# Optimization experiments

Hardware: AMD Instinct MI355X
Metric: run time of the kernel (lower is better)

The kernel has to match this reference:

```python
import jax, jax.numpy as jnp
import numpy as np

N = 100000        # nodes
E = 1600000       # directed edges (avg degree 16)
EMB = 32          # emb_hidden_dim
HID = 16          # hidden
Q = 0.25          # magnetic charge
NUM_SYMP = 15
BY = 4            # num_birthyear_disc


def _norm(edge_index, edge_weight):
    # Magnetic Laplacian, 'sym' normalization, lambda_max=2:
    # L_hat(u,v) = -deg^{-1/2}(u) * A_sym(u,v) * deg^{-1/2}(v) * exp(i*theta(u,v)),
    # theta = 2*pi*q*(A - A^T); diagonal of scaled L_hat is 0.
    src, dst = edge_index[0], edge_index[1]
    src2 = jnp.concatenate([src, dst])
    dst2 = jnp.concatenate([dst, src])
    sym_w = jnp.concatenate([edge_weight, edge_weight]) * 0.5
    theta = (2.0 * jnp.pi * Q) * jnp.concatenate([edge_weight, -edge_weight])
    deg = jax.ops.segment_sum(sym_w, dst2, num_segments=N)
    dinv = jnp.where(deg > 0, jax.lax.rsqrt(jnp.where(deg > 0, deg, 1.0)), 0.0)
    norm = dinv[src2] * sym_w * dinv[dst2]
    return src2, dst2, -norm * jnp.cos(theta), -norm * jnp.sin(theta)


def _cmatvec(src2, dst2, a_re, a_im, xr, xi):
    # complex sparse matvec: (A_re + i A_im)(x_re + i x_im)
    xr_s, xi_s = xr[src2], xi[src2]
    yr = jax.ops.segment_sum(a_re[:, None] * xr_s - a_im[:, None] * xi_s, dst2, num_segments=N)
    yi = jax.ops.segment_sum(a_re[:, None] * xi_s + a_im[:, None] * xr_s, dst2, num_segments=N)
    return yr, yi


def _magnet_conv(xr, xi, adj, W, b):
    # Chebyshev recursion T0=x, T1=L_hat x, T2=2 L_hat T1 - T0; out = sum_k T_k @ W[k] + b
    src2, dst2, a_re, a_im = adj
    out_r = xr @ W[0]
    out_i = xi @ W[0]
    t1r, t1i = _cmatvec(src2, dst2, a_re, a_im, xr, xi)
    out_r = out_r + t1r @ W[1]
    out_i = out_i + t1i @ W[1]
    t2r, t2i = _cmatvec(src2, dst2, a_re, a_im, t1r, t1i)
    t2r = 2.0 * t2r - xr
    t2i = 2.0 * t2i - xi
    out_r = out_r + t2r @ W[2]
    out_i = out_i + t2i @ W[2]
    return out_r + b, out_i + b


def setup_inputs() -> dict:
    key = jax.random.key(0)
    ks = jax.random.split(key, 12)
    birth = jax.random.randint(ks[0], (N,), 0, BY)
    gender = jax.random.randint(ks[1], (N,), 0, 2)
    symp = jax.random.randint(ks[2], (N, NUM_SYMP), 0, 3)
    x = jnp.concatenate([
        jax.nn.one_hot(birth, BY, dtype=jnp.int32),
        gender[:, None].astype(jnp.int32),
        symp.astype(jnp.int32),
    ], axis=1)  # [N, 20]
    edge_index = jax.random.randint(ks[3], (2, E), 0, N)
    edge_weight = jnp.ones((E,), jnp.float32)
    s = 0.1
    return {
        'x': x,
        'edge_index': edge_index,
        'edge_weight': edge_weight,
        'birth_tab': jax.random.normal(ks[4], (BY, EMB), jnp.float32) * s,
        'gender_tab': jax.random.normal(ks[5], (2, EMB), jnp.float32) * s,
        'symp_tab': jax.random.normal(ks[6], (NUM_SYMP, 3, EMB), jnp.float32) * s,
        'W1': jax.random.normal(ks[7], (3, EMB, HID), jnp.float32) * s,
        'b1': jnp.zeros((HID,), jnp.float32),
        'W2': jax.random.normal(ks[8], (3, HID, HID), jnp.float32) * s,
        'b2': jnp.zeros((HID,), jnp.float32),
        'Wc': jax.random.normal(ks[9], (2 * HID, 2 * HID), jnp.float32) * s,  # Conv1d k=1 (out,in)
        'bc': jnp.zeros((2 * HID,), jnp.float32),
        'Wl': jax.random.normal(ks[10], (2 * HID, 1), jnp.float32) * s,
        'bl': jnp.zeros((1,), jnp.float32),
    }


def reference(x, edge_index, edge_weight, birth_tab, gender_tab, symp_tab,
              W1, b1, W2, b2, Wc, bc, Wl, bl):
    # embedding gathers + mean fusion
    birth_idx = jnp.argmax(x[:, :BY] == 1, axis=1)
    birth_e = birth_tab[birth_idx]                              # [N, EMB]
    gender_e = gender_tab[x[:, BY]]                             # [N, EMB]
    symp_e = symp_tab[jnp.arange(NUM_SYMP)[None, :], x[:, -NUM_SYMP:]]  # [N, 15, EMB]
    feat = jnp.mean(symp_e, axis=1)
    h = (birth_e + gender_e + feat) / 3.0                       # [N, EMB]
    # complex Chebyshev spectral graph conv layers
    adj = _norm(edge_index, edge_weight)
    re, im = _magnet_conv(h, h, adj, W1, b1)
    re, im = _magnet_conv(re, im, adj, W2, b2)
    z = jnp.concatenate([re, im], axis=-1)                      # [N, 2*HID]
    z = z @ Wc.T + bc                                           # Conv1d kernel_size=1
    y = z @ Wl + bl                                             # Linear(2*HID, 1)
    return y[:, 0]
```

## Files before the change

kernel.cpp:

```cpp
#include <hip/hip_runtime.h>
#include <hip/hip_fp16.h>
#include <math.h>

static constexpr float PI2Q = 1.57079632679489662f;
#define CSH 9
#define CROWS 512
#define MAXKEY 256

__device__ __forceinline__ float2 h2f_bits(int b) {
  __half2 h = *reinterpret_cast<__half2*>(&b);
  return __half22float2(h);
}
__device__ __forceinline__ int f2h_bits(float a, float b) {
  __half2 h = __floats2half2_rn(a, b);
  return *reinterpret_cast<int*>(&h);
}

__global__ void k_weff(const float* __restrict__ Wc, const float* __restrict__ bc,
                       const float* __restrict__ Wl, const float* __restrict__ bl,
                       float* __restrict__ weff) {
  int k = threadIdx.x;
  if (k < 32) {
    float s = 0.f;
    #pragma unroll
    for (int j = 0; j < 32; ++j) s += Wc[j * 32 + k] * Wl[j];
    weff[k] = s;
  } else if (k == 32) {
    float s = 0.f;
    for (int j = 0; j < 32; ++j) s += bc[j] * Wl[j];
    weff[32] = s + bl[0];
  }
}

__global__ __launch_bounds__(256) void k_embed(
    const int* __restrict__ x, const float* __restrict__ btab,
    const float* __restrict__ gtab, const float* __restrict__ stab,
    const float* __restrict__ W1, const float* __restrict__ b1,
    float* __restrict__ PQ, __half2* __restrict__ PQh, float* __restrict__ o0, int n) {
  __shared__ float sm[3184];
  int tid = threadIdx.x;
  for (int t = tid; t < 1536; t += 256) sm[t] = W1[t];
  if (tid < 16) sm[1536 + tid] = b1[tid];
  for (int t = tid; t < 128; t += 256) sm[1552 + t] = btab[t];
  for (int t = tid; t < 64; t += 256) sm[1680 + t] = gtab[t];
  for (int t = tid; t < 1440; t += 256) sm[1744 + t] = stab[t];
  __syncthreads();
  int i = blockIdx.x * 256 + tid;
  if (i >= n) return;
  int xr[20];
  #pragma unroll
  for (int j = 0; j < 20; ++j) xr[j] = x[i * 20 + j];
  int bi = 0;
  #pragma unroll
  for (int j = 3; j >= 0; --j) if (xr[j] == 1) bi = j;
  int g = xr[4];
  float h[32];
  #pragma unroll
  for (int f = 0; f < 32; ++f) {
    float s = 0.f;
    #pragma unroll
    for (int j = 0; j < 15; ++j) s += sm[1744 + j * 96 + xr[5 + j] * 32 + f];
    h[f] = (sm[1552 + bi * 32 + f] + sm[1680 + g * 32 + f] + s * (1.f / 15.f)) * (1.f / 3.f);
  }
  #pragma unroll
  for (int f = 0; f < 16; ++f) {
    float o = sm[1536 + f], p = 0.f, q = 0.f;
    #pragma unroll
    for (int k = 0; k < 32; ++k) {
      float hk = h[k];
      o = fmaf(hk, sm[k * 16 + f], o);
      p = fmaf(hk, sm[512 + k * 16 + f], p);
      q = fmaf(hk, sm[1024 + k * 16 + f], q);
    }
    o0[i * 16 + f] = o;
    PQ[i * 32 + 2 * f] = p;
    PQ[i * 32 + 2 * f + 1] = q;
    PQh[(size_t)i * 16 + f] = __floats2half2_rn(p, q);
  }
}

__global__ __launch_bounds__(256) void k_rhist(const int* __restrict__ ei, int* __restrict__ rcnt,
                                               int E_) {
  __shared__ int h[MAXKEY * 8];
  int tid = threadIdx.x;
  for (int t = tid; t < MAXKEY * 8; t += 256) h[t] = 0;
  __syncthreads();
  int slot = tid & 7;
  int stride = gridDim.x * 256;
  for (int e = blockIdx.x * 256 + tid; e < E_; e += stride) {
    int s = ei[e], d = ei[E_ + e];
    atomicAdd(&h[(d >> CSH) * 8 + slot], 1);
    atomicAdd(&h[(s >> CSH) * 8 + slot], 1);
  }
  __syncthreads();
  for (int t = tid; t < MAXKEY; t += 256) {
    int sum = 0;
    #pragma unroll
    for (int j = 0; j < 8; ++j) sum += h[t * 8 + j];
    if (sum) atomicAdd(&rcnt[t], sum);
  }
}

__global__ void k_rbase(const int* __restrict__ rcnt, int* __restrict__ rbase, int* __restrict__ rcur,
                        int nkey) {
  if (threadIdx.x == 0) {
    int run = 0;
    for (int r = 0; r < nkey; ++r) { rbase[r] = run; rcur[r] = run; run += rcnt[r]; }
    rbase[nkey] = run;
  }
}

__global__ __launch_bounds__(256) void k_bucket(const int* __restrict__ ei, const float* __restrict__ ew,
                                                int* __restrict__ rcur, int* __restrict__ brow,
                                                int2* __restrict__ bsw, int E_) {
  __shared__ int lcnt[MAXKEY];
  __shared__ int gbase[MAXKEY];
  int tid = threadIdx.x;
  lcnt[tid] = 0;
  __syncthreads();
  int e0 = blockIdx.x * 2048;
  int s[8], d[8], wb[8], kA[8], kB[8], la[8], lb[8];
  #pragma unroll
  for (int j = 0; j < 8; ++j) {
    int e = e0 + j * 256 + tid;
    if (e < E_) {
      s[j] = ei[e]; d[j] = ei[E_ + e]; wb[j] = __float_as_int(ew[e]);
      kA[j] = d[j] >> CSH;
      kB[j] = s[j] >> CSH;
      la[j] = atomicAdd(&lcnt[kA[j]], 1);
      lb[j] = atomicAdd(&lcnt[kB[j]], 1);
    } else {
      kA[j] = -1; kB[j] = -1; s[j] = 0; d[j] = 0; wb[j] = 0; la[j] = 0; lb[j] = 0;
    }
  }
  __syncthreads();
  gbase[tid] = lcnt[tid] ? atomicAdd(&rcur[tid], lcnt[tid]) : 0;
  __syncthreads();
  #pragma unroll
  for (int j = 0; j < 8; ++j) {
    if (kA[j] >= 0) {
      int pA = gbase[kA[j]] + la[j];
      brow[pA] = d[j];
      bsw[pA] = make_int2(s[j], wb[j]);
      int pB = gbase[kB[j]] + lb[j];
      brow[pB] = s[j];
      bsw[pB] = make_int2(d[j] | (int)0x80000000, wb[j]);
    }
  }
}

__global__ __launch_bounds__(1024) void k_chunkdeg(const int* __restrict__ brow, const int2* __restrict__ bsw,
                                                   const int* __restrict__ rbase, int* __restrict__ rowp,
                                                   float* __restrict__ dinv, int n, int nkey) {
  __shared__ int hist[CROWS];
  __shared__ float wsum[CROWS];
  __shared__ int pref[CROWS];
  int c = blockIdx.x;
  int base = c << CSH;
  int rows = min(CROWS, n - base);
  int tid = threadIdx.x;
  if (tid < CROWS) { hist[tid] = 0; wsum[tid] = 0.f; }
  __syncthreads();
  int k0 = rbase[c], k1 = rbase[c + 1];
  for (int k = k0 + tid; k < k1; k += 1024) {
    int rl = brow[k] - base;
    atomicAdd(&hist[rl], 1);
    atomicAdd(&wsum[rl], __int_as_float(bsw[k].y));
  }
  __syncthreads();
  if (tid < CROWS) pref[tid] = hist[tid];
  __syncthreads();
  for (int off = 1; off < CROWS; off <<= 1) {
    int t = (tid < CROWS && tid >= off) ? pref[tid - off] : 0;
    __syncthreads();
    if (tid < CROWS) pref[tid] += t;
    __syncthreads();
  }
  if (tid < rows) {
    rowp[base + tid] = k0 + pref[tid] - hist[tid];
    float dg = 0.5f * wsum[tid];
    dinv[base + tid] = (dg > 0.f) ? rsqrtf(dg) : 0.f;
  }
  if (c == 0 && tid == 0) rowp[n] = rbase[nkey];
}

__global__ __launch_bounds__(1024) void k_chunkplace(const int* __restrict__ brow, const int2* __restrict__ bsw,
                                                     const int* __restrict__ rbase, const int* __restrict__ rowp,
                                                     const float* __restrict__ dinv, int2* __restrict__ recs,
                                                     int n) {
  __shared__ int cur[CROWS];
  __shared__ float dloc[CROWS];
  int c = blockIdx.x;
  int base = c << CSH;
  int rows = min(CROWS, n - base);
  int tid = threadIdx.x;
  if (tid < rows) { cur[tid] = rowp[base + tid]; dloc[tid] = dinv[base + tid]; }
  __syncthreads();
  int k0 = rbase[c], k1 = rbase[c + 1];
  for (int k = k0 + tid; k < k1; k += 1024) {
    int rl = brow[k] - base;
    int2 p = bsw[k];
    int s = p.x & 0x7fffffff;
    float w = __int_as_float(p.y);
    float nrm = dloc[rl] * 0.5f * w * dinv[s];
    float sn, cs;
    sincosf(PI2Q * w, &sn, &cs);
    float ar = -nrm * cs;
    float ai = (p.x < 0) ? nrm * sn : -nrm * sn;
    int pos = atomicAdd(&cur[rl], 1);
    recs[pos] = make_int2(p.x, f2h_bits(ar, ai));
  }
}

__global__ __launch_bounds__(256, 8) void k_hop_sym(
    const int* __restrict__ rowp, const int2* __restrict__ recs,
    const __half2* __restrict__ PQh, __half2* __restrict__ Uh, float* __restrict__ AB, int n) {
  int wid = (blockIdx.x * 256 + threadIdx.x) >> 6;
  if (wid >= n) return;
  int lane = threadIdx.x & 63;
  int fq = lane & 3, su = lane >> 2;
  int rs = rowp[wid], rend = rowp[wid + 1];
  float aA[4] = {0.f, 0.f, 0.f, 0.f}, aB[4] = {0.f, 0.f, 0.f, 0.f};
  float aC[4] = {0.f, 0.f, 0.f, 0.f}, aD[4] = {0.f, 0.f, 0.f, 0.f};
  const long long* rq = reinterpret_cast<const long long*>(recs);
  const int4* Pq = reinterpret_cast<const int4*>(PQh);
  for (int k = rs + su; k < rend; k += 16) {
    long long r0 = __builtin_nontemporal_load(rq + k);
    int s = ((int)r0) & 0x7fffffff;
    float2 a = h2f_bits((int)(r0 >> 32));
    float wm = a.x - a.y, wp = a.x + a.y;
    int4 v = Pq[(size_t)s * 4 + fq];
    float2 x0 = h2f_bits(v.x), x1 = h2f_bits(v.y), x2 = h2f_bits(v.z), x3 = h2f_bits(v.w);
    aA[0] = fmaf(wm, x0.x, aA[0]); aB[0] = fmaf(wp, x0.x, aB[0]);
    aC[0] = fmaf(wm, x0.y, aC[0]); aD[0] = fmaf(wp, x0.y, aD[0]);
    aA[1] = fmaf(wm, x1.x, aA[1]); aB[1] = fmaf(wp, x1.x, aB[1]);
    aC[1] = fmaf(wm, x1.y, aC[1]); aD[1] = fmaf(wp, x1.y, aD[1]);
    aA[2] = fmaf(wm, x2.x, aA[2]); aB[2] = fmaf(wp, x2.x, aB[2]);
    aC[2] = fmaf(wm, x2.y, aC[2]); aD[2] = fmaf(wp, x2.y, aD[2]);
    aA[3] = fmaf(wm, x3.x, aA[3]); aB[3] = fmaf(wp, x3.x, aB[3]);
    aC[3] = fmaf(wm, x3.y, aC[3]); aD[3] = fmaf(wp, x3.y, aD[3]);
  }
  #pragma unroll
  for (int j = 0; j < 4; ++j) {
    aA[j] += __shfl_xor(aA[j], 4); aA[j] += __shfl_xor(aA[j], 8);
    aA[j] += __shfl_xor(aA[j], 16); aA[j] += __shfl_xor(aA[j], 32);
    aB[j] += __shfl_xor(aB[j], 4); aB[j] += __shfl_xor(aB[j], 8);
    aB[j] += __shfl_xor(aB[j], 16); aB[j] += __shfl_xor(aB[j], 32);
    aC[j] += __shfl_xor(aC[j], 4); aC[j] += __shfl_xor(aC[j], 8);
    aC[j] += __shfl_xor(aC[j], 16); aC[j] += __shfl_xor(aC[j], 32);
    aD[j] += __shfl_xor(aD[j], 4); aD[j] += __shfl_xor(aD[j], 8);
    aD[j] += __shfl_xor(aD[j], 16); aD[j] += __shfl_xor(aD[j], 32);
  }
  if (lane < 4) {
    *reinterpret_cast<float4*>(AB + wid * 32 + 8 * fq) = make_float4(aA[0], aB[0], aA[1], aB[1]);
    *reinterpret_cast<float4*>(AB + wid * 32 + 8 * fq + 4) = make_float4(aA[2], aB[2], aA[3], aB[3]);
    int4 hv;
    hv.x = f2h_bits(aC[0], aD[0]); hv.y = f2h_bits(aC[1], aD[1]);
    hv.z = f2h_bits(aC[2], aD[2]); hv.w = f2h_bits(aC[3], aD[3]);
    *reinterpret_cast<int4*>(Uh + (size_t)wid * 16 + 4 * fq) = hv;
  }
}

template <int MODE>
__global__ __launch_bounds__(256, 8) void k_hop_full(
    const int* __restrict__ rowp, const int2* __restrict__ recs,
    const __half2* __restrict__ Xh, float* __restrict__ Y, __half2* __restrict__ Yh,
    const float* __restrict__ o0, const float* __restrict__ AB, const float* __restrict__ PQ,
    const float* __restrict__ D, const float* __restrict__ weff, int n) {
  int wid = (blockIdx.x * 256 + threadIdx.x) >> 6;
  if (wid >= n) return;
  int lane = threadIdx.x & 63;
  int fq = lane & 3, su = lane >> 2;
  int rs = rowp[wid], rend = rowp[wid + 1];
  float aR[4] = {0.f, 0.f, 0.f, 0.f}, aI[4] = {0.f, 0.f, 0.f, 0.f};
  const long long* rq = reinterpret_cast<const long long*>(recs);
  const int4* Xq = reinterpret_cast<const int4*>(Xh);
  for (int k = rs + su; k < rend; k += 16) {
    long long r0 = __builtin_nontemporal_load(rq + k);
    int s = ((int)r0) & 0x7fffffff;
    float2 a = h2f_bits((int)(r0 >> 32));
    int4 v = Xq[(size_t)s * 4 + fq];
    float2 x0 = h2f_bits(v.x), x1 = h2f_bits(v.y), x2 = h2f_bits(v.z), x3 = h2f_bits(v.w);
    aR[0] = fmaf(a.x, x0.x, aR[0]); aR[0] = fmaf(-a.y, x0.y, aR[0]);
    aI[0] = fmaf(a.x, x0.y, aI[0]); aI[0] = fmaf(a.y, x0.x, aI[0]);
    aR[1] = fmaf(a.x, x1.x, aR[1]); aR[1] = fmaf(-a.y, x1.y, aR[1]);
    aI[1] = fmaf(a.x, x1.y, aI[1]); aI[1] = fmaf(a.y, x1.x, aI[1]);
    aR[2] = fmaf(a.x, x2.x, aR[2]); aR[2] = fmaf(-a.y, x2.y, aR[2]);
    aI[2] = fmaf(a.x, x2.y, aI[2]); aI[2] = fmaf(a.y, x2.x, aI[2]);
    aR[3] = fmaf(a.x, x3.x, aR[3]); aR[3] = fmaf(-a.y, x3.y, aR[3]);
    aI[3] = fmaf(a.x, x3.y, aI[3]); aI[3] = fmaf(a.y, x3.x, aI[3]);
  }
  #pragma unroll
  for (int j = 0; j < 4; ++j) {
    aR[j] += __shfl_xor(aR[j], 4); aR[j] += __shfl_xor(aR[j], 8);
    aR[j] += __shfl_xor(aR[j], 16); aR[j] += __shfl_xor(aR[j], 32);
    aI[j] += __shfl_xor(aI[j], 4); aI[j] += __shfl_xor(aI[j], 8);
    aI[j] += __shfl_xor(aI[j], 16); aI[j] += __shfl_xor(aI[j], 32);
  }
  if (MODE == 2) {
    float c = 0.f;
    if (lane < 4) {
      float4 d0 = *reinterpret_cast<const float4*>(D + wid * 32 + 8 * fq);
      float4 d1 = *reinterpret_cast<const float4*>(D + wid * 32 + 8 * fq + 4);
      float4 w0 = *reinterpret_cast<const float4*>(weff + 4 * fq);
      float4 w1 = *reinterpret_cast<const float4*>(weff + 16 + 4 * fq);
      c  = (d0.x + 2.f * aR[0]) * w0.x + (d0.y + 2.f * aI[0]) * w1.x;
      c += (d0.z + 2.f * aR[1]) * w0.y + (d0.w + 2.f * aI[1]) * w1.y;
      c += (d1.x + 2.f * aR[2]) * w0.z + (d1.y + 2.f * aI[2]) * w1.z;
      c += (d1.z + 2.f * aR[3]) * w0.w + (d1.w + 2.f * aI[3]) * w1.w;
    }
    c += __shfl_xor(c, 1); c += __shfl_xor(c, 2);
    if (lane == 0) Y[wid] = c + weff[32];
  } else if (lane < 4) {
    if (MODE == 0) {
      *reinterpret_cast<float4*>(Y + wid * 32 + 8 * fq) = make_float4(aR[0], aI[0], aR[1], aI[1]);
      *reinterpret_cast<float4*>(Y + wid * 32 + 8 * fq + 4) = make_float4(aR[2], aI[2], aR[3], aI[3]);
    } else {
      float4 o = *reinterpret_cast<const float4*>(o0 + wid * 16 + 4 * fq);
      float4 ab0 = *reinterpret_cast<const float4*>(AB + wid * 32 + 8 * fq);
      float4 ab1 = *reinterpret_cast<const float4*>(AB + wid * 32 + 8 * fq + 4);
      float4 pq0 = *reinterpret_cast<const float4*>(PQ + wid * 32 + 8 * fq);
      float4 pq1 = *reinterpret_cast<const float4*>(PQ + wid * 32 + 8 * fq + 4);
      float zr0 = o.x + ab0.x + 2.f * aR[0] - pq0.y;
      float zi0 = o.x + ab0.y + 2.f * aI[0] - pq0.y;
      float zr1 = o.y + ab0.z + 2.f * aR[1] - pq0.w;
      float zi1 = o.y + ab0.w + 2.f * aI[1] - pq0.w;
      float zr2 = o.z + ab1.x + 2.f * aR[2] - pq1.y;
      float zi2 = o.z + ab1.y + 2.f * aI[2] - pq1.y;
      float zr3 = o.w + ab1.z + 2.f * aR[3] - pq1.w;
      float zi3 = o.w + ab1.w + 2.f * aI[3] - pq1.w;
      *reinterpret_cast<float4*>(Y + wid * 32 + 8 * fq) = make_float4(zr0, zi0, zr1, zi1);
      *reinterpret_cast<float4*>(Y + wid * 32 + 8 * fq + 4) = make_float4(zr2, zi2, zr3, zi3);
      int4 hv;
      hv.x = f2h_bits(zr0, zi0); hv.y = f2h_bits(zr1, zi1);
      hv.z = f2h_bits(zr2, zi2); hv.w = f2h_bits(zr3, zi3);
      *reinterpret_cast<int4*>(Yh + (size_t)wid * 16 + 4 * fq) = hv;
    }
  }
}

__global__ __launch_bounds__(256) void k_d2(const float* __restrict__ X2, const float* __restrict__ T1,
                                            const float* __restrict__ W2g, const float* __restrict__ b2g,
                                            __half2* __restrict__ U2h, float* __restrict__ D, int n) {
  __shared__ float sm[1040];
  int tid = threadIdx.x;
  for (int t = tid; t < 768; t += 256) sm[t] = W2g[t];
  if (tid < 16) sm[768 + tid] = b2g[tid];
  __syncthreads();
  if (tid < 256) sm[784 + tid] = sm[tid] - sm[512 + tid];
  __syncthreads();
  int i = blockIdx.x * 256 + tid;
  if (i >= n) return;
  float re[16], im[16], tr[16], ti[16];
  #pragma unroll
  for (int k = 0; k < 16; ++k) {
    float2 a = *reinterpret_cast<const float2*>(X2 + i * 32 + 2 * k);
    re[k] = a.x; im[k] = a.y;
    float2 b = *reinterpret_cast<const float2*>(T1 + i * 32 + 2 * k);
    tr[k] = b.x; ti[k] = b.y;
  }
  #pragma unroll
  for (int f = 0; f < 16; ++f) {
    float ur = 0.f, ui = 0.f;
    float dr = sm[768 + f], di = sm[768 + f];
    #pragma unroll
    for (int k = 0; k < 16; ++k) {
      float w2 = sm[512 + k * 16 + f];
      float w1 = sm[256 + k * 16 + f];
      float w02 = sm[784 + k * 16 + f];
      ur = fmaf(tr[k], w2, ur);
      ui = fmaf(ti[k], w2, ui);
      dr = fmaf(re[k], w02, dr); dr = fmaf(tr[k], w1, dr);
      di = fmaf(im[k], w02, di); di = fmaf(ti[k], w1, di);
    }
    U2h[(size_t)i * 16 + f] = __floats2half2_rn(ur, ui);
    *reinterpret_cast<float2*>(D + i * 32 + 2 * f) = make_float2(dr, di);
  }
}

extern "C" void kernel_launch(void* const* d_in, const int* in_sizes, int n_in,
                              void* d_out, int out_size, void* d_ws, size_t ws_size,
                              hipStream_t stream) {
  const int* x = (const int*)d_in[0];
  const int* ei = (const int*)d_in[1];
  const float* ew = (const float*)d_in[2];
  const float* btab = (const float*)d_in[3];
  const float* gtab = (const float*)d_in[4];
  const float* stab = (const float*)d_in[5];
  const float* W1 = (const float*)d_in[6];
  const float* b1 = (const float*)d_in[7];
  const float* W2 = (const float*)d_in[8];
  const float* b2 = (const float*)d_in[9];
  const float* Wc = (const float*)d_in[10];
  const float* bc = (const float*)d_in[11];
  const float* Wl = (const float*)d_in[12];
  const float* bl = (const float*)d_in[13];
  float* yout = (float*)d_out;

  const int N_ = in_sizes[0] / 20;
  const int E_ = in_sizes[1] / 2;
  const int M_ = 2 * E_;
  const int nkey = (N_ + CROWS - 1) >> CSH;

  size_t off = 0;
  auto take = [&](size_t bytes) -> void* {
    void* p = (char*)d_ws + off;
    off += (bytes + 255) & ~(size_t)255;
    return p;
  };
  float* PQ   = (float*)take((size_t)N_ * 32 * 4);
  float* o0   = (float*)take((size_t)N_ * 16 * 4);
  float* Ubuf = (float*)take((size_t)N_ * 32 * 4);
  float* ABuf = (float*)take((size_t)N_ * 32 * 4);
  float* X2   = (float*)take((size_t)N_ * 32 * 4);
  float* dinv = (float*)take((size_t)N_ * 4);
  int* rowp   = (int*)take((size_t)(N_ + 1) * 4);
  float* weff = (float*)take(64 * 4);
  int* rcnt   = (int*)take(MAXKEY * 4);
  int* rbase  = (int*)take((MAXKEY + 1) * 4);
  int* rcur   = (int*)take(MAXKEY * 4);
  int* brow   = (int*)take((size_t)M_ * 4);
  int2* bsw   = (int2*)take((size_t)M_ * 8);
  int2* recs  = (int2*)take((size_t)M_ * 8);
  (void)ws_size; (void)n_in; (void)out_size;

  __half2* PQh = (__half2*)brow;
  __half2* Uh  = (__half2*)((char*)brow + (size_t)N_ * 64);
  __half2* X2h = (__half2*)bsw;
  __half2* U2h = (__half2*)((char*)bsw + (size_t)N_ * 64);

  int nbN = (N_ + 255) / 256;
  int nbH = (N_ + 3) / 4;
  int nbB = (E_ + 2047) / 2048;

  hipMemsetAsync(rcnt, 0, MAXKEY * 4, stream);

  k_weff<<<1, 64, 0, stream>>>(Wc, bc, Wl, bl, weff);

  k_rhist<<<512, 256, 0, stream>>>(ei, rcnt, E_);
  k_rbase<<<1, 64, 0, stream>>>(rcnt, rbase, rcur, nkey);
  k_bucket<<<nbB, 256, 0, stream>>>(ei, ew, rcur, brow, bsw, E_);
  k_chunkdeg<<<nkey, 1024, 0, stream>>>(brow, bsw, rbase, rowp, dinv, N_, nkey);
  k_chunkplace<<<nkey, 1024, 0, stream>>>(brow, bsw, rbase, rowp, dinv, recs, N_);

  k_embed<<<nbN, 256, 0, stream>>>(x, btab, gtab, stab, W1, b1, PQ, PQh, o0, N_);

  k_hop_sym<<<nbH, 256, 0, stream>>>(rowp, recs, PQh, Uh, ABuf, N_);
  k_hop_full<1><<<nbH, 256, 0, stream>>>(rowp, recs, Uh, X2, X2h, o0, ABuf, PQ,
                                         nullptr, nullptr, N_);
  k_hop_full<0><<<nbH, 256, 0, stream>>>(rowp, recs, X2h, Ubuf, nullptr, nullptr,
                                         nullptr, nullptr, nullptr, nullptr, N_);
  k_d2<<<nbN, 256, 0, stream>>>(X2, Ubuf, W2, b2, U2h, ABuf, N_);
  k_hop_full<2><<<nbH, 256, 0, stream>>>(rowp, recs, U2h, yout, nullptr, nullptr,
                                         nullptr, nullptr, ABuf, weff, N_);
}
```

Measured before the change: 452.2 us.

## Make hop kernels persistent with software-prefetched edge records for next row

Converts the four SpMM hop kernels from one-wavefront-per-row launches into a persistent grid of 2048 blocks where each wavefront strides over rows. While the current row is processed, it prefetches the next row's rowp bounds and first three edge records, and it issues the first three feature gathers of each row together to raise memory-level parallelism. The aim is to hide gather latency and launch/tail overhead. The cost is extra registers, masked dummy gathers for short rows, and fewer resident wavefronts if the grid is too small for the device.

```diff
diff --git a/kernel.cpp b/kernel.cpp
--- a/kernel.cpp
+++ b/kernel.cpp
@@ -6,6 +6,7 @@
 #define CSH 9
 #define CROWS 512
 #define MAXKEY 256
+#define HOPB 2048
 
 __device__ __forceinline__ float2 h2f_bits(int b) {
   __half2 h = *reinterpret_cast<__half2*>(&b);
@@ -214,50 +215,99 @@
 
 __global__ __launch_bounds__(256, 8) void k_hop_sym(
     const int* __restrict__ rowp, const int2* __restrict__ recs,
-    const __half2* __restrict__ PQh, __half2* __restrict__ Uh, float* __restrict__ AB, int n) {
-  int wid = (blockIdx.x * 256 + threadIdx.x) >> 6;
-  if (wid >= n) return;
+    const __half2* __restrict__ PQh, __half2* __restrict__ Uh, float* __restrict__ AB,
+    int n, int M, int W) {
+  int w = (blockIdx.x * 256 + threadIdx.x) >> 6;
+  if (w >= n) return;
   int lane = threadIdx.x & 63;
   int fq = lane & 3, su = lane >> 2;
-  int rs = rowp[wid], rend = rowp[wid + 1];
-  float aA[4] = {0.f, 0.f, 0.f, 0.f}, aB[4] = {0.f, 0.f, 0.f, 0.f};
-  float aC[4] = {0.f, 0.f, 0.f, 0.f}, aD[4] = {0.f, 0.f, 0.f, 0.f};
   const long long* rq = reinterpret_cast<const long long*>(recs);
   const int4* Pq = reinterpret_cast<const int4*>(PQh);
-  for (int k = rs + su; k < rend; k += 16) {
-    long long r0 = __builtin_nontemporal_load(rq + k);
-    int s = ((int)r0) & 0x7fffffff;
-    float2 a = h2f_bits((int)(r0 >> 32));
-    float wm = a.x - a.y, wp = a.x + a.y;
-    int4 v = Pq[(size_t)s * 4 + fq];
-    float2 x0 = h2f_bits(v.x), x1 = h2f_bits(v.y), x2 = h2f_bits(v.z), x3 = h2f_bits(v.w);
-    aA[0] = fmaf(wm, x0.x, aA[0]); aB[0] = fmaf(wp, x0.x, aB[0]);
-    aC[0] = fmaf(wm, x0.y, aC[0]); aD[0] = fmaf(wp, x0.y, aD[0]);
-    aA[1] = fmaf(wm, x1.x, aA[1]); aB[1] = fmaf(wp, x1.x, aB[1]);
-    aC[1] = fmaf(wm, x1.y, aC[1]); aD[1] = fmaf(wp, x1.y, aD[1]);
-    aA[2] = fmaf(wm, x2.x, aA[2]); aB[2] = fmaf(wp, x2.x, aB[2]);
-    aC[2] = fmaf(wm, x2.y, aC[2]); aD[2] = fmaf(wp, x2.y, aD[2]);
-    aA[3] = fmaf(wm, x3.x, aA[3]); aB[3] = fmaf(wp, x3.x, aB[3]);
-    aC[3] = fmaf(wm, x3.y, aC[3]); aD[3] = fmaf(wp, x3.y, aD[3]);
-  }
-  #pragma unroll
-  for (int j = 0; j < 4; ++j) {
-    aA[j] += __shfl_xor(aA[j], 4); aA[j] += __shfl_xor(aA[j], 8);
-    aA[j] += __shfl_xor(aA[j], 16); aA[j] += __shfl_xor(aA[j], 32);
-    aB[j] += __shfl_xor(aB[j], 4); aB[j] += __shfl_xor(aB[j], 8);
-    aB[j] += __shfl_xor(aB[j], 16); aB[j] += __shfl_xor(aB[j], 32);
-    aC[j] += __shfl_xor(aC[j], 4); aC[j] += __shfl_xor(aC[j], 8);
-    aC[j] += __shfl_xor(aC[j], 16); aC[j] += __shfl_xor(aC[j], 32);
-    aD[j] += __shfl_xor(aD[j], 4); aD[j] += __shfl_xor(aD[j], 8);
-    aD[j] += __shfl_xor(aD[j], 16); aD[j] += __shfl_xor(aD[j], 32);
-  }
-  if (lane < 4) {
-    *reinterpret_cast<float4*>(AB + wid * 32 + 8 * fq) = make_float4(aA[0], aB[0], aA[1], aB[1]);
-    *reinterpret_cast<float4*>(AB + wid * 32 + 8 * fq + 4) = make_float4(aA[2], aB[2], aA[3], aB[3]);
-    int4 hv;
-    hv.x = f2h_bits(aC[0], aD[0]); hv.y = f2h_bits(aC[1], aD[1]);
-    hv.z = f2h_bits(aC[2], aD[2]); hv.w = f2h_bits(aC[3], aD[3]);
-    *reinterpret_cast<int4*>(Uh + (size_t)wid * 16 + 4 * fq) = hv;
+  int Mm1 = M - 1;
+
+  int r = w;
+  int rs = rowp[r], re = rowp[r + 1];
+  int k0 = rs + su;
+  long long c0 = __builtin_nontemporal_load(rq + min(k0, Mm1));
+  long long c1 = __builtin_nontemporal_load(rq + min(k0 + 16, Mm1));
+  long long c2 = __builtin_nontemporal_load(rq + min(k0 + 32, Mm1));
+
+  while (true) {
+    int rn = r + W;
+    int nrs = 0, nre = 0;
+    if (rn < n) { nrs = rowp[rn]; nre = rowp[rn + 1]; }
+
+    int s0 = ((int)c0) & 0x7fffffff;
+    int s1 = ((int)c1) & 0x7fffffff;
+    int s2 = ((int)c2) & 0x7fffffff;
+    float2 a0 = h2f_bits((int)(c0 >> 32));
+    float2 a1 = h2f_bits((int)(c1 >> 32));
+    float2 a2 = h2f_bits((int)(c2 >> 32));
+    if (k0 >= re)      { a0 = make_float2(0.f, 0.f); }
+    if (k0 + 16 >= re) { a1 = make_float2(0.f, 0.f); s1 = s0; }
+    if (k0 + 32 >= re) { a2 = make_float2(0.f, 0.f); s2 = s0; }
+
+    int4 g0 = Pq[(size_t)s0 * 4 + fq];
+    int4 g1 = Pq[(size_t)s1 * 4 + fq];
+    int4 g2 = Pq[(size_t)s2 * 4 + fq];
+
+    long long n0 = 0, n1 = 0, n2 = 0;
+    int nk0 = nrs + su;
+    if (rn < n) {
+      n0 = __builtin_nontemporal_load(rq + min(nk0, Mm1));
+      n1 = __builtin_nontemporal_load(rq + min(nk0 + 16, Mm1));
+      n2 = __builtin_nontemporal_load(rq + min(nk0 + 32, Mm1));
+    }
+
+    float aA[4] = {0.f, 0.f, 0.f, 0.f}, aB[4] = {0.f, 0.f, 0.f, 0.f};
+    float aC[4] = {0.f, 0.f, 0.f, 0.f}, aD[4] = {0.f, 0.f, 0.f, 0.f};
+    #define SYM_FMA(aa, vv)                                                              \
+    {                                                                                    \
+      float wm = aa.x - aa.y, wp = aa.x + aa.y;                                          \
+      float2 x0 = h2f_bits(vv.x), x1 = h2f_bits(vv.y), x2 = h2f_bits(vv.z), x3 = h2f_bits(vv.w); \
+      aA[0] = fmaf(wm, x0.x, aA[0]); aB[0] = fmaf(wp, x0.x, aB[0]);                      \
+      aC[0] = fmaf(wm, x0.y, aC[0]); aD[0] = fmaf(wp, x0.y, aD[0]);                      \
+      aA[1] = fmaf(wm, x1.x, aA[1]); aB[1] = fmaf(wp, x1.x, aB[1]);                      \
+      aC[1] = fmaf(wm, x1.y, aC[1]); aD[1] = fmaf(wp, x1.y, aD[1]);                      \
+      aA[2] = fmaf(wm, x2.x, aA[2]); aB[2] = fmaf(wp, x2.x, aB[2]);                      \
+      aC[2] = fmaf(wm, x2.y, aC[2]); aD[2] = fmaf(wp, x2.y, aD[2]);                      \
+      aA[3] = fmaf(wm, x3.x, aA[3]); aB[3] = fmaf(wp, x3.x, aB[3]);                      \
+      aC[3] = fmaf(wm, x3.y, aC[3]); aD[3] = fmaf(wp, x3.y, aD[3]);                      \
+    }
+    SYM_FMA(a0, g0);
+    SYM_FMA(a1, g1);
+    SYM_FMA(a2, g2);
+    for (int k = rs + 48 + su; k < re; k += 16) {
+      long long rr = __builtin_nontemporal_load(rq + k);
+      int ss = ((int)rr) & 0x7fffffff;
+      float2 aa = h2f_bits((int)(rr >> 32));
+      int4 gg = Pq[(size_t)ss * 4 + fq];
+      SYM_FMA(aa, gg);
+    }
+    #undef SYM_FMA
+
+    #pragma unroll
+    for (int j = 0; j < 4; ++j) {
+      aA[j] += __shfl_xor(aA[j], 4); aA[j] += __shfl_xor(aA[j], 8);
+      aA[j] += __shfl_xor(aA[j], 16); aA[j] += __shfl_xor(aA[j], 32);
+      aB[j] += __shfl_xor(aB[j], 4); aB[j] += __shfl_xor(aB[j], 8);
+      aB[j] += __shfl_xor(aB[j], 16); aB[j] += __shfl_xor(aB[j], 32);
+      aC[j] += __shfl_xor(aC[j], 4); aC[j] += __shfl_xor(aC[j], 8);
+      aC[j] += __shfl_xor(aC[j], 16); aC[j] += __shfl_xor(aC[j], 32);
+      aD[j] += __shfl_xor(aD[j], 4); aD[j] += __shfl_xor(aD[j], 8);
+      aD[j] += __shfl_xor(aD[j], 16); aD[j] += __shfl_xor(aD[j], 32);
+    }
+    if (lane < 4) {
+      *reinterpret_cast<float4*>(AB + r * 32 + 8 * fq) = make_float4(aA[0], aB[0], aA[1], aB[1]);
+      *reinterpret_cast<float4*>(AB + r * 32 + 8 * fq + 4) = make_float4(aA[2], aB[2], aA[3], aB[3]);
+      int4 hv;
+      hv.x = f2h_bits(aC[0], aD[0]); hv.y = f2h_bits(aC[1], aD[1]);
+      hv.z = f2h_bits(aC[2], aD[2]); hv.w = f2h_bits(aC[3], aD[3]);
+      *reinterpret_cast<int4*>(Uh + (size_t)r * 16 + 4 * fq) = hv;
+    }
+    if (rn >= n) break;
+    r = rn; rs = nrs; re = nre; k0 = nk0;
+    c0 = n0; c1 = n1; c2 = n2;
   }
 }
 
@@ -266,76 +316,124 @@
     const int* __restrict__ rowp, const int2* __restrict__ recs,
     const __half2* __restrict__ Xh, float* __restrict__ Y, __half2* __restrict__ Yh,
     const float* __restrict__ o0, const float* __restrict__ AB, const float* __restrict__ PQ,
-    const float* __restrict__ D, const float* __restrict__ weff, int n) {
-  int wid = (blockIdx.x * 256 + threadIdx.x) >> 6;
-  if (wid >= n) return;
+    const float* __restrict__ D, const float* __restrict__ weff, int n, int M, int W) {
+  int w = (blockIdx.x * 256 + threadIdx.x) >> 6;
+  if (w >= n) return;
   int lane = threadIdx.x & 63;
   int fq = lane & 3, su = lane >> 2;
-  int rs = rowp[wid], rend = rowp[wid + 1];
-  float aR[4] = {0.f, 0.f, 0.f, 0.f}, aI[4] = {0.f, 0.f, 0.f, 0.f};
   const long long* rq = reinterpret_cast<const long long*>(recs);
   const int4* Xq = reinterpret_cast<const int4*>(Xh);
-  for (int k = rs + su; k < rend; k += 16) {
-    long long r0 = __builtin_nontemporal_load(rq + k);
-    int s = ((int)r0) & 0x7fffffff;
-    float2 a = h2f_bits((int)(r0 >> 32));
-    int4 v = Xq[(size_t)s * 4 + fq];
-    float2 x0 = h2f_bits(v.x), x1 = h2f_bits(v.y), x2 = h2f_bits(v.z), x3 = h2f_bits(v.w);
-    aR[0] = fmaf(a.x, x0.x, aR[0]); aR[0] = fmaf(-a.y, x0.y, aR[0]);
-    aI[0] = fmaf(a.x, x0.y, aI[0]); aI[0] = fmaf(a.y, x0.x, aI[0]);
-    aR[1] = fmaf(a.x, x1.x, aR[1]); aR[1] = fmaf(-a.y, x1.y, aR[1]);
-    aI[1] = fmaf(a.x, x1.y, aI[1]); aI[1] = fmaf(a.y, x1.x, aI[1]);
-    aR[2] = fmaf(a.x, x2.x, aR[2]); aR[2] = fmaf(-a.y, x2.y, aR[2]);
-    aI[2] = fmaf(a.x, x2.y, aI[2]); aI[2] = fmaf(a.y, x2.x, aI[2]);
-    aR[3] = fmaf(a.x, x3.x, aR[3]); aR[3] = fmaf(-a.y, x3.y, aR[3]);
-    aI[3] = fmaf(a.x, x3.y, aI[3]); aI[3] = fmaf(a.y, x3.x, aI[3]);
-  }
-  #pragma unroll
-  for (int j = 0; j < 4; ++j) {
-    aR[j] += __shfl_xor(aR[j], 4); aR[j] += __shfl_xor(aR[j], 8);
-    aR[j] += __shfl_xor(aR[j], 16); aR[j] += __shfl_xor(aR[j], 32);
-    aI[j] += __shfl_xor(aI[j], 4); aI[j] += __shfl_xor(aI[j], 8);
-    aI[j] += __shfl_xor(aI[j], 16); aI[j] += __shfl_xor(aI[j], 32);
-  }
-  if (MODE == 2) {
-    float c = 0.f;
-    if (lane < 4) {
-      float4 d0 = *reinterpret_cast<const float4*>(D + wid * 32 + 8 * fq);
-      float4 d1 = *reinterpret_cast<const float4*>(D + wid * 32 + 8 * fq + 4);
-      float4 w0 = *reinterpret_cast<const float4*>(weff + 4 * fq);
-      float4 w1 = *reinterpret_cast<const float4*>(weff + 16 + 4 * fq);
-      c  = (d0.x + 2.f * aR[0]) * w0.x + (d0.y + 2.f * aI[0]) * w1.x;
-      c += (d0.z + 2.f * aR[1]) * w0.y + (d0.w + 2.f * aI[1]) * w1.y;
-      c += (d1.x + 2.f * aR[2]) * w0.z + (d1.y + 2.f * aI[2]) * w1.z;
-      c += (d1.z + 2.f * aR[3]) * w0.w + (d1.w + 2.f * aI[3]) * w1.w;
-    }
-    c += __shfl_xor(c, 1); c += __shfl_xor(c, 2);
-    if (lane == 0) Y[wid] = c + weff[32];
-  } else if (lane < 4) {
-    if (MODE == 0) {
-      *reinterpret_cast<float4*>(Y + wid * 32 + 8 * fq) = make_float4(aR[0], aI[0], aR[1], aI[1]);
-      *reinterpret_cast<float4*>(Y + wid * 32 + 8 * fq + 4) = make_float4(aR[2], aI[2], aR[3], aI[3]);
-    } else {
-      float4 o = *reinterpret_cast<const float4*>(o0 + wid * 16 + 4 * fq);
-      float4 ab0 = *reinterpret_cast<const float4*>(AB + wid * 32 + 8 * fq);
-      float4 ab1 = *reinterpret_cast<const float4*>(AB + wid * 32 + 8 * fq + 4);
-      float4 pq0 = *reinterpret_cast<const float4*>(PQ + wid * 32 + 8 * fq);
-      float4 pq1 = *reinterpret_cast<const float4*>(PQ + wid * 32 + 8 * fq + 4);
-      float zr0 = o.x + ab0.x + 2.f * aR[0] - pq0.y;
-      float zi0 = o.x + ab0.y + 2.f * aI[0] - pq0.y;
-      float zr1 = o.y + ab0.z + 2.f * aR[1] - pq0.w;
-      float zi1 = o.y + ab0.w + 2.f * aI[1] - pq0.w;
-      float zr2 = o.z + ab1.x + 2.f * aR[2] - pq1.y;
-      float zi2 = o.z + ab1.y + 2.f * aI[2] - pq1.y;
-      float zr3 = o.w + ab1.z + 2.f * aR[3] - pq1.w;
-      float zi3 = o.w + ab1.w + 2.f * aI[3] - pq1.w;
-      *reinterpret_cast<float4*>(Y + wid * 32 + 8 * fq) = make_float4(zr0, zi0, zr1, zi1);
-      *reinterpret_cast<float4*>(Y + wid * 32 + 8 * fq + 4) = make_float4(zr2, zi2, zr3, zi3);
-      int4 hv;
-      hv.x = f2h_bits(zr0, zi0); hv.y = f2h_bits(zr1, zi1);
-      hv.z = f2h_bits(zr2, zi2); hv.w = f2h_bits(zr3, zi3);
-      *reinterpret_cast<int4*>(Yh + (size_t)wid * 16 + 4 * fq) = hv;
-    }
+  int Mm1 = M - 1;
+
+  int r = w;
+  int rs = rowp[r], re = rowp[r + 1];
+  int k0 = rs + su;
+  long long c0 = __builtin_nontemporal_load(rq + min(k0, Mm1));
+  long long c1 = __builtin_nontemporal_load(rq + min(k0 + 16, Mm1));
+  long long c2 = __builtin_nontemporal_load(rq + min(k0 + 32, Mm1));
+
+  while (true) {
+    int rn = r + W;
+    int nrs = 0, nre = 0;
+    if (rn < n) { nrs = rowp[rn]; nre = rowp[rn + 1]; }
+
+    int s0 = ((int)c0) & 0x7fffffff;
+    int s1 = ((int)c1) & 0x7fffffff;
+    int s2 = ((int)c2) & 0x7fffffff;
+    float2 a0 = h2f_bits((int)(c0 >> 32));
+    float2 a1 = h2f_bits((int)(c1 >> 32));
+    float2 a2 = h2f_bits((int)(c2 >> 32));
+    if (k0 >= re)      { a0 = make_float2(0.f, 0.f); }
+    if (k0 + 16 >= re) { a1 = make_float2(0.f, 0.f); s1 = s0; }
+    if (k0 + 32 >= re) { a2 = make_float2(0.f, 0.f); s2 = s0; }
+
+    int4 g0 = Xq[(size_t)s0 * 4 + fq];
+    int4 g1 = Xq[(size_t)s1 * 4 + fq];
+    int4 g2 = Xq[(size_t)s2 * 4 + fq];
+
+    long long n0 = 0, n1 = 0, n2 = 0;
+    int nk0 = nrs + su;
+    if (rn < n) {
+      n0 = __builtin_nontemporal_load(rq + min(nk0, Mm1));
+      n1 = __builtin_nontemporal_load(rq + min(nk0 + 16, Mm1));
+      n2 = __builtin_nontemporal_load(rq + min(nk0 + 32, Mm1));
+    }
+
+    float aR[4] = {0.f, 0.f, 0.f, 0.f}, aI[4] = {0.f, 0.f, 0.f, 0.f};
+    #define FULL_FMA(aa, vv)                                                             \
+    {                                                                                    \
+      float2 x0 = h2f_bits(vv.x), x1 = h2f_bits(vv.y), x2 = h2f_bits(vv.z), x3 = h2f_bits(vv.w); \
+      aR[0] = fmaf(aa.x, x0.x, aR[0]); aR[0] = fmaf(-aa.y, x0.y, aR[0]);                 \
+      aI[0] = fmaf(aa.x, x0.y, aI[0]); aI[0] = fmaf(aa.y, x0.x, aI[0]);                  \
+      aR[1] = fmaf(aa.x, x1.x, aR[1]); aR[1] = fmaf(-aa.y, x1.y, aR[1]);                 \
+      aI[1] = fmaf(aa.x, x1.y, aI[1]); aI[1] = fmaf(aa.y, x1.x, aI[1]);                  \
+      aR[2] = fmaf(aa.x, x2.x, aR[2]); aR[2] = fmaf(-aa.y, x2.y, aR[2]);                 \
+      aI[2] = fmaf(aa.x, x2.y, aI[2]); aI[2] = fmaf(aa.y, x2.x, aI[2]);                  \
+      aR[3] = fmaf(aa.x, x3.x, aR[3]); aR[3] = fmaf(-aa.y, x3.y, aR[3]);                 \
+      aI[3] = fmaf(aa.x, x3.y, aI[3]); aI[3] = fmaf(aa.y, x3.x, aI[3]);                  \
+    }
+    FULL_FMA(a0, g0);
+    FULL_FMA(a1, g1);
+    FULL_FMA(a2, g2);
+    for (int k = rs + 48 + su; k < re; k += 16) {
+      long long rr = __builtin_nontemporal_load(rq + k);
+      int ss = ((int)rr) & 0x7fffffff;
+      float2 aa = h2f_bits((int)(rr >> 32));
+      int4 gg = Xq[(size_t)ss * 4 + fq];
+      FULL_FMA(aa, gg);
+    }
+    #undef FULL_FMA
+
+    #pragma unroll
+    for (int j = 0; j < 4; ++j) {
+      aR[j] += __shfl_xor(aR[j], 4); aR[j] += __shfl_xor(aR[j], 8);
+      aR[j] += __shfl_xor(aR[j], 16); aR[j] += __shfl_xor(aR[j], 32);
+      aI[j] += __shfl_xor(aI[j], 4); aI[j] += __shfl_xor(aI[j], 8);
+      aI[j] += __shfl_xor(aI[j], 16); aI[j] += __shfl_xor(aI[j], 32);
+    }
+    if (MODE == 2) {
+      float c = 0.f;
+      if (lane < 4) {
+        float4 d0 = *reinterpret_cast<const float4*>(D + r * 32 + 8 * fq);
+        float4 d1 = *reinterpret_cast<const float4*>(D + r * 32 + 8 * fq + 4);
+        float4 w0 = *reinterpret_cast<const float4*>(weff + 4 * fq);
+        float4 w1 = *reinterpret_cast<const float4*>(weff + 16 + 4 * fq);
+        c  = (d0.x + 2.f * aR[0]) * w0.x + (d0.y + 2.f * aI[0]) * w1.x;
+        c += (d0.z + 2.f * aR[1]) * w0.y + (d0.w + 2.f * aI[1]) * w1.y;
+        c += (d1.x + 2.f * aR[2]) * w0.z + (d1.y + 2.f * aI[2]) * w1.z;
+        c += (d1.z + 2.f * aR[3]) * w0.w + (d1.w + 2.f * aI[3]) * w1.w;
+      }
+      c += __shfl_xor(c, 1); c += __shfl_xor(c, 2);
+      if (lane == 0) Y[r] = c + weff[32];
+    } else if (lane < 4) {
+      if (MODE == 0) {
+        *reinterpret_cast<float4*>(Y + r * 32 + 8 * fq) = make_float4(aR[0], aI[0], aR[1], aI[1]);
+        *reinterpret_cast<float4*>(Y + r * 32 + 8 * fq + 4) = make_float4(aR[2], aI[2], aR[3], aI[3]);
+      } else {
+        float4 o = *reinterpret_cast<const float4*>(o0 + r * 16 + 4 * fq);
+        float4 ab0 = *reinterpret_cast<const float4*>(AB + r * 32 + 8 * fq);
+        float4 ab1 = *reinterpret_cast<const float4*>(AB + r * 32 + 8 * fq + 4);
+        float4 pq0 = *reinterpret_cast<const float4*>(PQ + r * 32 + 8 * fq);
+        float4 pq1 = *reinterpret_cast<const float4*>(PQ + r * 32 + 8 * fq + 4);
+        float zr0 = o.x + ab0.x + 2.f * aR[0] - pq0.y;
+        float zi0 = o.x + ab0.y + 2.f * aI[0] - pq0.y;
+        float zr1 = o.y + ab0.z + 2.f * aR[1] - pq0.w;
+        float zi1 = o.y + ab0.w + 2.f * aI[1] - pq0.w;
+        float zr2 = o.z + ab1.x + 2.f * aR[2] - pq1.y;
+        float zi2 = o.z + ab1.y + 2.f * aI[2] - pq1.y;
+        float zr3 = o.w + ab1.z + 2.f * aR[3] - pq1.w;
+        float zi3 = o.w + ab1.w + 2.f * aI[3] - pq1.w;
+        *reinterpret_cast<float4*>(Y + r * 32 + 8 * fq) = make_float4(zr0, zi0, zr1, zi1);
+        *reinterpret_cast<float4*>(Y + r * 32 + 8 * fq + 4) = make_float4(zr2, zi2, zr3, zi3);
+        int4 hv;
+        hv.x = f2h_bits(zr0, zi0); hv.y = f2h_bits(zr1, zi1);
+        hv.z = f2h_bits(zr2, zi2); hv.w = f2h_bits(zr3, zi3);
+        *reinterpret_cast<int4*>(Yh + (size_t)r * 16 + 4 * fq) = hv;
+      }
+    }
+    if (rn >= n) break;
+    r = rn; rs = nrs; re = nre; k0 = nk0;
+    c0 = n0; c1 = n1; c2 = n2;
   }
 }
 
@@ -430,8 +528,8 @@
   __half2* U2h = (__half2*)((char*)bsw + (size_t)N_ * 64);
 
   int nbN = (N_ + 255) / 256;
-  int nbH = (N_ + 3) / 4;
   int nbB = (E_ + 2047) / 2048;
+  const int W = HOPB * 4;
 
   hipMemsetAsync(rcnt, 0, MAXKEY * 4, stream);
 
@@ -445,12 +543,12 @@
 
   k_embed<<<nbN, 256, 0, stream>>>(x, btab, gtab, stab, W1, b1, PQ, PQh, o0, N_);
 
-  k_hop_sym<<<nbH, 256, 0, stream>>>(rowp, recs, PQh, Uh, ABuf, N_);
-  k_hop_full<1><<<nbH, 256, 0, stream>>>(rowp, recs, Uh, X2, X2h, o0, ABuf, PQ,
-                                         nullptr, nullptr, N_);
-  k_hop_full<0><<<nbH, 256, 0, stream>>>(rowp, recs, X2h, Ubuf, nullptr, nullptr,
-                                         nullptr, nullptr, nullptr, nullptr, N_);
+  k_hop_sym<<<HOPB, 256, 0, stream>>>(rowp, recs, PQh, Uh, ABuf, N_, M_, W);
+  k_hop_full<1><<<HOPB, 256, 0, stream>>>(rowp, recs, Uh, X2, X2h, o0, ABuf, PQ,
+                                          nullptr, nullptr, N_, M_, W);
+  k_hop_full<0><<<HOPB, 256, 0, stream>>>(rowp, recs, X2h, Ubuf, nullptr, nullptr,
+                                          nullptr, nullptr, nullptr, nullptr, N_, M_, W);
   k_d2<<<nbN, 256, 0, stream>>>(X2, Ubuf, W2, b2, U2h, ABuf, N_);
-  k_hop_full<2><<<nbH, 256, 0, stream>>>(rowp, recs, U2h, yout, nullptr, nullptr,
-                                         nullptr, nullptr, ABuf, weff, N_);
-}
+  k_hop_full<2><<<HOPB, 256, 0, stream>>>(rowp, recs, U2h, yout, nullptr, nullptr,
+                                          nullptr, nullptr, ABuf, weff, N_, M_, W);
+}
```

Measured after the change: 472.4 us. +4.5%, slower.
